# Performance work log

Measured on AMD Instinct MI355X. Metric: run time of the kernel, lower is better.

## Reference

```python
import jax, jax.numpy as jnp
import numpy as np

D_MODEL = 2048
N_HEADS = 16
HEAD_DIM = D_MODEL // N_HEADS  # 128
B, T = 2, 2048


def setup_inputs() -> dict:
    key = jax.random.key(0)
    ks = jax.random.split(key, 5)
    s = 0.02
    x = jax.random.normal(ks[0], (B, T, D_MODEL), dtype=jnp.float32)
    # weights stored as [in, out] (math-equivalent to torch Linear's W.T)
    Wq = jax.random.normal(ks[1], (D_MODEL, D_MODEL), dtype=jnp.float32) * s
    Wk = jax.random.normal(ks[2], (D_MODEL, HEAD_DIM), dtype=jnp.float32) * s
    Wv = jax.random.normal(ks[3], (D_MODEL, HEAD_DIM), dtype=jnp.float32) * s
    Wo = jax.random.normal(ks[4], (D_MODEL, D_MODEL), dtype=jnp.float32) * s
    return {"x": x, "Wq": Wq, "Wk": Wk, "Wv": Wv, "Wo": Wo}


def reference(x, Wq, Wk, Wv, Wo):
    Bx, Tx, Dx = x.shape
    scale = HEAD_DIM ** -0.5
    # q: (B, H, T, hd); k, v: single shared head (B, T, hd)
    q = (x @ Wq).reshape(Bx, Tx, N_HEADS, HEAD_DIM).transpose(0, 2, 1, 3)
    k = x @ Wk  # (B, T, hd)
    v = x @ Wv  # (B, T, hd)
    # scores: (B, H, T, T) -- shared KV head broadcast across query heads
    attn = jnp.einsum('bhqd,bkd->bhqk', q, k) * scale
    causal = jnp.triu(jnp.ones((Tx, Tx), dtype=bool), k=1)  # True = masked
    attn = jnp.where(causal[None, None], -jnp.inf, attn)
    weights = jax.nn.softmax(attn, axis=-1)
    weights = jnp.nan_to_num(weights)
    out = jnp.einsum('bhqk,bkd->bhqd', weights, v)  # (B, H, T, hd)
    out = out.transpose(0, 2, 1, 3).reshape(Bx, Tx, Dx)
    return out @ Wo
```

## Files before the change

### kernel.cpp

```cpp
#include <hip/hip_runtime.h>

typedef __bf16 bf16x8 __attribute__((ext_vector_type(8)));
typedef float f32x4 __attribute__((ext_vector_type(4)));

__device__ inline void gload16(const __bf16* g, __bf16* l) {
  __builtin_amdgcn_global_load_lds(
      (const __attribute__((address_space(1))) unsigned int*)g,
      (__attribute__((address_space(3))) unsigned int*)l, 16, 0, 0);
}

__global__ __launch_bounds__(256) void conv_bf16(
    const float* __restrict__ in, __bf16* __restrict__ out)
{
  size_t i = ((size_t)blockIdx.x * 256 + threadIdx.x) * 8;
  float4 a = *(const float4*)&in[i];
  float4 b = *(const float4*)&in[i + 4];
  bf16x8 h;
  h[0] = (__bf16)a.x; h[1] = (__bf16)a.y; h[2] = (__bf16)a.z; h[3] = (__bf16)a.w;
  h[4] = (__bf16)b.x; h[5] = (__bf16)b.y; h[6] = (__bf16)b.z; h[7] = (__bf16)b.w;
  *(bf16x8*)&out[i] = h;
}

__global__ __launch_bounds__(256) void transpose_w(
    const float* __restrict__ W, __bf16* __restrict__ WT, int Kd, int Nd)
{
  __shared__ __bf16 Ts[64 * 72];
  const int tid = threadIdx.x;
  const int c0 = blockIdx.x * 64, r0 = blockIdx.y * 64;
#pragma unroll
  for (int i = 0; i < 4; i++) {
    int row = (tid >> 4) + i * 16, cv = (tid & 15) * 4;
    float4 w = *(const float4*)&W[(size_t)(r0 + row) * Nd + c0 + cv];
    Ts[(cv + 0) * 72 + row] = (__bf16)w.x;
    Ts[(cv + 1) * 72 + row] = (__bf16)w.y;
    Ts[(cv + 2) * 72 + row] = (__bf16)w.z;
    Ts[(cv + 3) * 72 + row] = (__bf16)w.w;
  }
  __syncthreads();
#pragma unroll
  for (int i = 0; i < 4; i++) {
    int n = (tid >> 4) + i * 16, kseg = (tid & 15) * 4;
    *(uint2*)&WT[(size_t)(c0 + n) * Kd + r0 + kseg] = *(uint2*)&Ts[n * 72 + kseg];
  }
}

__global__ __launch_bounds__(256) void gemm_qkv(
    const __bf16* __restrict__ A, const __bf16* __restrict__ WqT,
    const __bf16* __restrict__ WkT, const __bf16* __restrict__ WvT,
    __bf16* __restrict__ Cq, __bf16* __restrict__ Ck, __bf16* __restrict__ Cv)
{
  __shared__ __align__(16) __bf16 Asl[128 * 32];
  __shared__ __align__(16) __bf16 Bsl[128 * 32];
  const int tid = threadIdx.x, wave = tid >> 6, lane = tid & 63;
  const int quad = lane >> 4, l16 = lane & 15;
  const int nb = blockIdx.x, m0 = blockIdx.y * 128;
  const __bf16* BT; __bf16* C; int ldC, c0;
  if (nb < 16)       { BT = WqT + (size_t)nb * 128 * 2048; C = Cq; ldC = 2048; c0 = nb * 128; }
  else if (nb == 16) { BT = WkT; C = Ck; ldC = 128; c0 = 0; }
  else               { BT = WvT; C = Cv; ldC = 128; c0 = 0; }
  const int wm = (wave >> 1) * 64, wn = (wave & 1) * 64;
  const int lrow = lane >> 2, lseg = (lane & 3) * 8;

  f32x4 acc[4][4];
#pragma unroll
  for (int i = 0; i < 4; i++)
#pragma unroll
    for (int j = 0; j < 4; j++) acc[i][j] = (f32x4){0.f, 0.f, 0.f, 0.f};

  for (int k0 = 0; k0 < 2048; k0 += 32) {
    __syncthreads();
#pragma unroll
    for (int c = 0; c < 2; c++) {
      int ch = wave * 2 + c;
      gload16(&A[(size_t)(m0 + ch * 16 + lrow) * 2048 + k0 + lseg], &Asl[ch * 512]);
      gload16(&BT[(size_t)(ch * 16 + lrow) * 2048 + k0 + lseg], &Bsl[ch * 512]);
    }
    __syncthreads();

    bf16x8 af[4], bf[4];
#pragma unroll
    for (int i = 0; i < 4; i++)
      af[i] = *(const bf16x8*)&Asl[(wm + i * 16 + l16) * 32 + quad * 8];
#pragma unroll
    for (int i = 0; i < 4; i++)
      bf[i] = *(const bf16x8*)&Bsl[(wn + i * 16 + l16) * 32 + quad * 8];
#pragma unroll
    for (int mi = 0; mi < 4; mi++)
#pragma unroll
      for (int ni = 0; ni < 4; ni++)
        acc[mi][ni] = __builtin_amdgcn_mfma_f32_16x16x32_bf16(
            af[mi], bf[ni], acc[mi][ni], 0, 0, 0);
  }

#pragma unroll
  for (int mi = 0; mi < 4; mi++)
#pragma unroll
    for (int ni = 0; ni < 4; ni++)
#pragma unroll
      for (int r = 0; r < 4; r++) {
        int row = m0 + wm + mi * 16 + quad * 4 + r;
        int col = c0 + wn + ni * 16 + l16;
        C[(size_t)row * ldC + col] = (__bf16)acc[mi][ni][r];
      }
}

__global__ __launch_bounds__(256) void gemm_out_bt(
    const __bf16* __restrict__ A, const __bf16* __restrict__ BT,
    float* __restrict__ Cp)
{
  __shared__ __align__(16) __bf16 Asl[128 * 32];
  __shared__ __align__(16) __bf16 Bsl[128 * 32];
  const int tid = threadIdx.x, wave = tid >> 6, lane = tid & 63;
  const int quad = lane >> 4, l16 = lane & 15;
  const int n0 = blockIdx.x * 128, m0 = blockIdx.y * 128;
  const int wm = (wave >> 1) * 64, wn = (wave & 1) * 64;
  const int lrow = lane >> 2, lseg = (lane & 3) * 8;

  f32x4 acc[4][4];
#pragma unroll
  for (int i = 0; i < 4; i++)
#pragma unroll
    for (int j = 0; j < 4; j++) acc[i][j] = (f32x4){0.f, 0.f, 0.f, 0.f};

  for (int k0 = 0; k0 < 2048; k0 += 32) {
    __syncthreads();
#pragma unroll
    for (int c = 0; c < 2; c++) {
      int ch = wave * 2 + c;
      gload16(&A[(size_t)(m0 + ch * 16 + lrow) * 2048 + k0 + lseg], &Asl[ch * 512]);
      gload16(&BT[(size_t)(n0 + ch * 16 + lrow) * 2048 + k0 + lseg], &Bsl[ch * 512]);
    }
    __syncthreads();

    bf16x8 af[4], bf[4];
#pragma unroll
    for (int i = 0; i < 4; i++)
      af[i] = *(const bf16x8*)&Asl[(wm + i * 16 + l16) * 32 + quad * 8];
#pragma unroll
    for (int i = 0; i < 4; i++)
      bf[i] = *(const bf16x8*)&Bsl[(wn + i * 16 + l16) * 32 + quad * 8];
#pragma unroll
    for (int mi = 0; mi < 4; mi++)
#pragma unroll
      for (int ni = 0; ni < 4; ni++)
        acc[mi][ni] = __builtin_amdgcn_mfma_f32_16x16x32_bf16(
            af[mi], bf[ni], acc[mi][ni], 0, 0, 0);
  }

#pragma unroll
  for (int mi = 0; mi < 4; mi++)
#pragma unroll
    for (int ni = 0; ni < 4; ni++)
#pragma unroll
      for (int r = 0; r < 4; r++) {
        int row = m0 + wm + mi * 16 + quad * 4 + r;
        int col = n0 + wn + ni * 16 + l16;
        Cp[(size_t)row * 2048 + col] = acc[mi][ni][r];
      }
}

__global__ __launch_bounds__(256) void gemm_out_f32b(
    const __bf16* __restrict__ A, const float* __restrict__ B,
    float* __restrict__ Cp)
{
  __shared__ __align__(16) __bf16 Asl[128 * 32];
  __shared__ __align__(16) __bf16 BsT[128 * 32];
  const int tid = threadIdx.x, wave = tid >> 6, lane = tid & 63;
  const int quad = lane >> 4, l16 = lane & 15;
  const int n0 = blockIdx.x * 128, m0 = blockIdx.y * 128;
  const int wm = (wave >> 1) * 64, wn = (wave & 1) * 64;
  const int lrow = lane >> 2, lseg = (lane & 3) * 8;
  const int kg = (tid >> 5) * 4, ng = (tid & 31) * 4;

  f32x4 acc[4][4];
#pragma unroll
  for (int i = 0; i < 4; i++)
#pragma unroll
    for (int j = 0; j < 4; j++) acc[i][j] = (f32x4){0.f, 0.f, 0.f, 0.f};

  for (int k0 = 0; k0 < 2048; k0 += 32) {
    __syncthreads();
#pragma unroll
    for (int c = 0; c < 2; c++) {
      int ch = wave * 2 + c;
      gload16(&A[(size_t)(m0 + ch * 16 + lrow) * 2048 + k0 + lseg], &Asl[ch * 512]);
    }
    __bf16 h[4][4];
#pragma unroll
    for (int i = 0; i < 4; i++) {
      float4 w = *(const float4*)&B[(size_t)(k0 + kg + i) * 2048 + n0 + ng];
      h[i][0] = (__bf16)w.x; h[i][1] = (__bf16)w.y;
      h[i][2] = (__bf16)w.z; h[i][3] = (__bf16)w.w;
    }
#pragma unroll
    for (int j = 0; j < 4; j++) {
      int n = ng + j;
      int pb = ((kg >> 3) + (n >> 2)) & 3;
      __bf16 o4[4] = {h[0][j], h[1][j], h[2][j], h[3][j]};
      *(uint2*)&BsT[n * 32 + pb * 8 + (kg & 7)] = *(uint2*)o4;
    }
    __syncthreads();

    bf16x8 af[4], bf[4];
#pragma unroll
    for (int i = 0; i < 4; i++)
      af[i] = *(const bf16x8*)&Asl[(wm + i * 16 + l16) * 32 + quad * 8];
#pragma unroll
    for (int i = 0; i < 4; i++) {
      int n = wn + i * 16 + l16;
      int pb = (quad + (n >> 2)) & 3;
      bf[i] = *(const bf16x8*)&BsT[n * 32 + pb * 8];
    }
#pragma unroll
    for (int mi = 0; mi < 4; mi++)
#pragma unroll
      for (int ni = 0; ni < 4; ni++)
        acc[mi][ni] = __builtin_amdgcn_mfma_f32_16x16x32_bf16(
            af[mi], bf[ni], acc[mi][ni], 0, 0, 0);
  }

#pragma unroll
  for (int mi = 0; mi < 4; mi++)
#pragma unroll
    for (int ni = 0; ni < 4; ni++)
#pragma unroll
      for (int r = 0; r < 4; r++) {
        int row = m0 + wm + mi * 16 + quad * 4 + r;
        int col = n0 + wn + ni * 16 + l16;
        Cp[(size_t)row * 2048 + col] = acc[mi][ni][r];
      }
}

#define KS_LD 136
#define VT_LD 72
#define PR_LD 72

__global__ __launch_bounds__(256) void mqa_attn_mfma(
    const __bf16* Q, const __bf16* __restrict__ Km,
    const __bf16* __restrict__ Vm, __bf16* O)
{
  __shared__ __align__(16) __bf16 Ks[64 * KS_LD];
  __shared__ __align__(16) __bf16 VsT[128 * VT_LD];
  __shared__ __align__(16) __bf16 Pr[4][32 * PR_LD];

  const int tid = threadIdx.x, wave = tid >> 6, lane = tid & 63;
  const int quad = lane >> 4, l16 = lane & 15;
  const int t = blockIdx.x >> 1, bat = blockIdx.x & 1;
  const int hg = blockIdx.y & 3, flip = blockIdx.y >> 2;
  const int qt = flip ? (63 - t) : t;
  const int h = hg * 4 + wave;
  const int q0 = qt * 32;
  const size_t qgrow = (size_t)bat * 2048 + q0;
  const float SCL2 = 0.08838834764831845f * 1.4426950408889634f;

  bf16x8 qf[2][4];
#pragma unroll
  for (int mi = 0; mi < 2; mi++)
#pragma unroll
    for (int ks = 0; ks < 4; ks++)
      qf[mi][ks] = *(const bf16x8*)(Q + (qgrow + mi * 16 + l16) * 2048 +
                                    h * 128 + ks * 32 + quad * 8);

  bf16x8 ones;
#pragma unroll
  for (int i = 0; i < 8; i++) ones[i] = (__bf16)1.0f;

  f32x4 oa[2][8];
#pragma unroll
  for (int mi = 0; mi < 2; mi++)
#pragma unroll
    for (int nt = 0; nt < 8; nt++) oa[mi][nt] = (f32x4){0.f, 0.f, 0.f, 0.f};
  f32x4 lacc[2];
  lacc[0] = (f32x4){0.f, 0.f, 0.f, 0.f};
  lacc[1] = (f32x4){0.f, 0.f, 0.f, 0.f};

  const __bf16* Kb = Km + (size_t)bat * 2048 * 128;
  const __bf16* Vb = Vm + (size_t)bat * 2048 * 128;
  const int qmax = q0 + 31;

  for (int sc = 0; sc <= qmax; sc += 64) {
    __syncthreads();
#pragma unroll
    for (int i = 0; i < 4; i++) {
      int v = tid + i * 256;
      int row = v >> 4, dseg = (v & 15) * 8;
      int kr = sc + row; if (kr > 2047) kr = 2047;
      *(bf16x8*)&Ks[row * KS_LD + dseg] =
          *(const bf16x8*)&Kb[(size_t)kr * 128 + dseg];
    }
#pragma unroll
    for (int i = 0; i < 2; i++) {
      int g = tid + i * 256;
      int dg = (g & 31) * 4, kg2 = (g >> 5) * 4;
      union { uint2 u; unsigned short s[4]; } a[4], o;
#pragma unroll
      for (int i2 = 0; i2 < 4; i2++) {
        int kr = sc + kg2 + i2; if (kr > 2047) kr = 2047;
        a[i2].u = *(const uint2*)&Vb[(size_t)kr * 128 + dg];
      }
#pragma unroll
      for (int j = 0; j < 4; j++) {
        int d = dg + j;
        int pb = ((kg2 >> 3) + (d >> 2)) & 7;
        o.s[0] = a[0].s[j]; o.s[1] = a[1].s[j];
        o.s[2] = a[2].s[j]; o.s[3] = a[3].s[j];
        *(uint2*)&VsT[d * VT_LD + pb * 8 + (kg2 & 7)] = o.u;
      }
    }
    __syncthreads();

    f32x4 sf[2][4];
#pragma unroll
    for (int mi = 0; mi < 2; mi++)
#pragma unroll
      for (int kt = 0; kt < 4; kt++) sf[mi][kt] = (f32x4){0.f, 0.f, 0.f, 0.f};
#pragma unroll
    for (int ks = 0; ks < 4; ks++)
#pragma unroll
      for (int kt = 0; kt < 4; kt++) {
        bf16x8 kf = *(const bf16x8*)&Ks[(kt * 16 + l16) * KS_LD + ks * 32 + quad * 8];
        sf[0][kt] = __builtin_amdgcn_mfma_f32_16x16x32_bf16(kf, qf[0][ks], sf[0][kt], 0, 0, 0);
        sf[1][kt] = __builtin_amdgcn_mfma_f32_16x16x32_bf16(kf, qf[1][ks], sf[1][kt], 0, 0, 0);
      }

    __bf16* prw = Pr[wave];
    if (sc + 64 > q0) {
#pragma unroll
      for (int mi = 0; mi < 2; mi++) {
        int qrow = q0 + mi * 16 + l16;
#pragma unroll
        for (int kt = 0; kt < 4; kt++) {
          int kbase = sc + kt * 16 + quad * 4;
          __bf16 h4[4];
#pragma unroll
          for (int r = 0; r < 4; r++) {
            float p = (kbase + r <= qrow) ? exp2f(sf[mi][kt][r] * SCL2) : 0.f;
            h4[r] = (__bf16)p;
          }
          *(uint2*)&prw[(mi * 16 + l16) * PR_LD + kt * 16 + quad * 4] = *(uint2*)h4;
        }
      }
    } else {
#pragma unroll
      for (int mi = 0; mi < 2; mi++)
#pragma unroll
        for (int kt = 0; kt < 4; kt++) {
          __bf16 h4[4];
#pragma unroll
          for (int r = 0; r < 4; r++) h4[r] = (__bf16)exp2f(sf[mi][kt][r] * SCL2);
          *(uint2*)&prw[(mi * 16 + l16) * PR_LD + kt * 16 + quad * 4] = *(uint2*)h4;
        }
    }

#pragma unroll
    for (int ks2 = 0; ks2 < 2; ks2++) {
      bf16x8 pf0 = *(const bf16x8*)&prw[(l16) * PR_LD + ks2 * 32 + quad * 8];
      bf16x8 pf1 = *(const bf16x8*)&prw[(16 + l16) * PR_LD + ks2 * 32 + quad * 8];
      lacc[0] = __builtin_amdgcn_mfma_f32_16x16x32_bf16(pf0, ones, lacc[0], 0, 0, 0);
      lacc[1] = __builtin_amdgcn_mfma_f32_16x16x32_bf16(pf1, ones, lacc[1], 0, 0, 0);
#pragma unroll
      for (int nt = 0; nt < 8; nt++) {
        int d = nt * 16 + l16;
        int pb = ((ks2 * 4 + quad) + (d >> 2)) & 7;
        bf16x8 vf = *(const bf16x8*)&VsT[d * VT_LD + pb * 8];
        oa[0][nt] = __builtin_amdgcn_mfma_f32_16x16x32_bf16(pf0, vf, oa[0][nt], 0, 0, 0);
        oa[1][nt] = __builtin_amdgcn_mfma_f32_16x16x32_bf16(pf1, vf, oa[1][nt], 0, 0, 0);
      }
    }
  }

#pragma unroll
  for (int mi = 0; mi < 2; mi++)
#pragma unroll
    for (int r = 0; r < 4; r++) {
      float inv = 1.f / lacc[mi][r];
      size_t row = qgrow + mi * 16 + quad * 4 + r;
#pragma unroll
      for (int nt = 0; nt < 8; nt++)
        O[row * 2048 + h * 128 + nt * 16 + l16] = (__bf16)(oa[mi][nt][r] * inv);
    }
}

extern "C" void kernel_launch(void* const* d_in, const int* in_sizes, int n_in,
                              void* d_out, int out_size, void* d_ws, size_t ws_size,
                              hipStream_t stream) {
  const float* x  = (const float*)d_in[0];
  const float* Wq = (const float*)d_in[1];
  const float* Wk = (const float*)d_in[2];
  const float* Wv = (const float*)d_in[3];
  const float* Wo = (const float*)d_in[4];
  float* out = (float*)d_out;

  __bf16* q   = (__bf16*)d_ws;
  __bf16* WoT = (__bf16*)((char*)d_ws + 16777216);
  const bool have_wot = ws_size >= (size_t)(16777216 + 8388608);

  char* ob = (char*)d_out;
  __bf16* xb  = (__bf16*)(ob);
  __bf16* WqT = (__bf16*)(ob + 16777216);
  __bf16* WkT = (__bf16*)(ob + 25165824);
  __bf16* WvT = (__bf16*)(ob + 25690112);
  __bf16* kb  = (__bf16*)(ob + 26214400);
  __bf16* vb  = (__bf16*)(ob + 27262976);

  dim3 blk(256);
  conv_bf16<<<4096, blk, 0, stream>>>(x, xb);
  transpose_w<<<dim3(32, 32), blk, 0, stream>>>(Wq, WqT, 2048, 2048);
  transpose_w<<<dim3(2, 32), blk, 0, stream>>>(Wk, WkT, 2048, 128);
  transpose_w<<<dim3(2, 32), blk, 0, stream>>>(Wv, WvT, 2048, 128);
  if (have_wot)
    transpose_w<<<dim3(32, 32), blk, 0, stream>>>(Wo, WoT, 2048, 2048);
  gemm_qkv<<<dim3(18, 32), blk, 0, stream>>>(xb, WqT, WkT, WvT, q, kb, vb);
  mqa_attn_mfma<<<dim3(64, 8, 1), blk, 0, stream>>>(q, kb, vb, q);
  if (have_wot)
    gemm_out_bt<<<dim3(16, 32), blk, 0, stream>>>(q, WoT, out);
  else
    gemm_out_f32b<<<dim3(16, 32), blk, 0, stream>>>(q, Wo, out);
}
```

Baseline: 298.2 us.

## Double-buffer K via async global-to-LDS loads and prefetch V in attention loop

The attention kernel now double-buffers the K tile in LDS, issuing the next chunk with global_load_lds DMA, and uses an XOR-swizzled unpadded layout in place of row padding. V for the next chunk is loaded into registers during compute and transposed into LDS after it. This is meant to hide global-memory latency behind the QK and PV MFMA work. Launch bounds now request two blocks per CU, which raises LDS use and register pressure and adds an extra barrier per iteration.

```diff
diff --git a/kernel.cpp b/kernel.cpp
--- a/kernel.cpp
+++ b/kernel.cpp
@@ -231,15 +231,14 @@
       }
 }
 
-#define KS_LD 136
 #define VT_LD 72
 #define PR_LD 72
 
-__global__ __launch_bounds__(256) void mqa_attn_mfma(
+__global__ __launch_bounds__(256, 2) void mqa_attn_mfma(
     const __bf16* Q, const __bf16* __restrict__ Km,
     const __bf16* __restrict__ Vm, __bf16* O)
 {
-  __shared__ __align__(16) __bf16 Ks[64 * KS_LD];
+  __shared__ __align__(16) __bf16 Ks[2][64 * 128];
   __shared__ __align__(16) __bf16 VsT[128 * VT_LD];
   __shared__ __align__(16) __bf16 Pr[4][32 * PR_LD];
 
@@ -277,37 +276,66 @@
   const __bf16* Kb = Km + (size_t)bat * 2048 * 128;
   const __bf16* Vb = Vm + (size_t)bat * 2048 * 128;
   const int qmax = q0 + 31;
-
-  for (int sc = 0; sc <= qmax; sc += 64) {
-    __syncthreads();
-#pragma unroll
-    for (int i = 0; i < 4; i++) {
-      int v = tid + i * 256;
-      int row = v >> 4, dseg = (v & 15) * 8;
-      int kr = sc + row; if (kr > 2047) kr = 2047;
-      *(bf16x8*)&Ks[row * KS_LD + dseg] =
-          *(const bf16x8*)&Kb[(size_t)kr * 128 + dseg];
-    }
-#pragma unroll
-    for (int i = 0; i < 2; i++) {
-      int g = tid + i * 256;
-      int dg = (g & 31) * 4, kg2 = (g >> 5) * 4;
-      union { uint2 u; unsigned short s[4]; } a[4], o;
-#pragma unroll
-      for (int i2 = 0; i2 < 4; i2++) {
-        int kr = sc + kg2 + i2; if (kr > 2047) kr = 2047;
-        a[i2].u = *(const uint2*)&Vb[(size_t)kr * 128 + dg];
-      }
-#pragma unroll
-      for (int j = 0; j < 4; j++) {
-        int d = dg + j;
-        int pb = ((kg2 >> 3) + (d >> 2)) & 7;
-        o.s[0] = a[0].s[j]; o.s[1] = a[1].s[j];
-        o.s[2] = a[2].s[j]; o.s[3] = a[3].s[j];
-        *(uint2*)&VsT[d * VT_LD + pb * 8 + (kg2 & 7)] = o.u;
-      }
-    }
-    __syncthreads();
+  const int nch = (qmax >> 6) + 1;
+
+  size_t koff[4];
+#pragma unroll
+  for (int p = 0; p < 4; p++) {
+    int row = wave * 16 + p * 4 + (lane >> 4);
+    int dbs = (lane & 15) ^ (row & 7);
+    koff[p] = (size_t)row * 128 + (size_t)dbs * 8;
+  }
+  int kswz[4];
+#pragma unroll
+  for (int ks = 0; ks < 4; ks++)
+    kswz[ks] = (((ks << 2) | quad) ^ (l16 & 7)) << 3;
+  const int vdg = (tid & 31) * 4;
+  const int vkgA = (tid >> 5) * 4;
+  uint2 va[2][4];
+
+#define ISSUE_K(Kc, buf)                                                     \
+  {                                                                          \
+    _Pragma("unroll") for (int p = 0; p < 4; p++)                            \
+        gload16((Kc) + koff[p], &Ks[buf][(wave * 4 + p) * 512]);             \
+  }
+#define LOAD_V(Vc)                                                           \
+  {                                                                          \
+    _Pragma("unroll") for (int i = 0; i < 2; i++)                            \
+        _Pragma("unroll") for (int r = 0; r < 4; r++)                        \
+            va[i][r] =                                                       \
+        *(const uint2*)&(Vc)[(size_t)(vkgA + i * 32 + r) * 128 + vdg];       \
+  }
+#define WRITE_V()                                                            \
+  {                                                                          \
+    _Pragma("unroll") for (int i = 0; i < 2; i++) {                          \
+      int kg2 = vkgA + i * 32;                                               \
+      _Pragma("unroll") for (int j = 0; j < 4; j++) {                        \
+        int d = vdg + j;                                                     \
+        int pb = ((kg2 >> 3) + (d >> 2)) & 7;                                \
+        union { uint2 u; unsigned short s[4]; } o;                           \
+        o.s[0] = ((const unsigned short*)&va[i][0])[j];                      \
+        o.s[1] = ((const unsigned short*)&va[i][1])[j];                      \
+        o.s[2] = ((const unsigned short*)&va[i][2])[j];                      \
+        o.s[3] = ((const unsigned short*)&va[i][3])[j];                      \
+        *(uint2*)&VsT[d * VT_LD + pb * 8 + (kg2 & 7)] = o.u;                 \
+      }                                                                      \
+    }                                                                        \
+  }
+
+  ISSUE_K(Kb, 0);
+  LOAD_V(Vb);
+  WRITE_V();
+  __syncthreads();
+
+  for (int c = 0; c < nch; ++c) {
+    const int sc = c << 6;
+    const __bf16* Ksb = Ks[c & 1];
+    const bool pf = (c + 1 < nch);
+
+    if (pf) {
+      ISSUE_K(Kb + (size_t)(sc + 64) * 128, (c & 1) ^ 1);
+      LOAD_V(Vb + (size_t)(sc + 64) * 128);
+    }
 
     f32x4 sf[2][4];
 #pragma unroll
@@ -318,7 +346,7 @@
     for (int ks = 0; ks < 4; ks++)
 #pragma unroll
       for (int kt = 0; kt < 4; kt++) {
-        bf16x8 kf = *(const bf16x8*)&Ks[(kt * 16 + l16) * KS_LD + ks * 32 + quad * 8];
+        bf16x8 kf = *(const bf16x8*)&Ksb[(kt * 16 + l16) * 128 + kswz[ks]];
         sf[0][kt] = __builtin_amdgcn_mfma_f32_16x16x32_bf16(kf, qf[0][ks], sf[0][kt], 0, 0, 0);
         sf[1][kt] = __builtin_amdgcn_mfma_f32_16x16x32_bf16(kf, qf[1][ks], sf[1][kt], 0, 0, 0);
       }
@@ -367,6 +395,12 @@
         oa[1][nt] = __builtin_amdgcn_mfma_f32_16x16x32_bf16(pf1, vf, oa[1][nt], 0, 0, 0);
       }
     }
+
+    if (pf) {
+      __syncthreads();
+      WRITE_V();
+      __syncthreads();
+    }
   }
 
 #pragma unroll
@@ -379,6 +413,9 @@
       for (int nt = 0; nt < 8; nt++)
         O[row * 2048 + h * 128 + nt * 16 + l16] = (__bf16)(oa[mi][nt][r] * inv);
     }
+#undef ISSUE_K
+#undef LOAD_V
+#undef WRITE_V
 }
 
 extern "C" void kernel_launch(void* const* d_in, const int* in_sizes, int n_in,
```

After: 296.0 us. No clear change (-0.7%).

## Split long causal attention tiles across two blocks and merge partials

Applied to the files above, without the earlier changes.

Query tiles in the second half of the sequence, which have the most causal KV chunks, are each split into two blocks that process half the chunks. This shortens the longest blocks and spreads work over more blocks. The first half writes fp32 partial outputs and row sums into reused scratch in the output buffer. The second half writes unnormalized bf16 partials, and a new combine kernel sums them and normalizes. The change also adds a launch-bounds occupancy hint and an extra launch, and rounding the unnormalized partial to bf16 before the merge may cost a little precision.

```diff
diff --git a/kernel.cpp b/kernel.cpp
--- a/kernel.cpp
+++ b/kernel.cpp
@@ -235,9 +235,10 @@
 #define VT_LD 72
 #define PR_LD 72
 
-__global__ __launch_bounds__(256) void mqa_attn_mfma(
+__global__ __launch_bounds__(256, 3) void mqa_attn_mfma(
     const __bf16* Q, const __bf16* __restrict__ Km,
-    const __bf16* __restrict__ Vm, __bf16* O)
+    const __bf16* __restrict__ Vm, __bf16* O,
+    float* __restrict__ Oacc, float* __restrict__ Lp)
 {
   __shared__ __align__(16) __bf16 Ks[64 * KS_LD];
   __shared__ __align__(16) __bf16 VsT[128 * VT_LD];
@@ -245,14 +246,26 @@
 
   const int tid = threadIdx.x, wave = tid >> 6, lane = tid & 63;
   const int quad = lane >> 4, l16 = lane & 15;
-  const int t = blockIdx.x >> 1, bat = blockIdx.x & 1;
-  const int hg = blockIdx.y & 3, flip = blockIdx.y >> 2;
-  const int qt = flip ? (63 - t) : t;
+  const int bx = blockIdx.x;
+  int qt, half, split;
+  if (bx < 64) { split = 1; qt = 63 - (bx >> 1); half = bx & 1; }
+  else         { split = 0; qt = 95 - bx; half = 1; }
+  const int hg = blockIdx.y & 3, bat = blockIdx.y >> 2;
   const int h = hg * 4 + wave;
   const int q0 = qt * 32;
   const size_t qgrow = (size_t)bat * 2048 + q0;
   const float SCL2 = 0.08838834764831845f * 1.4426950408889634f;
 
+  const int nch = (qt >> 1) + 1;
+  int cbeg, cend;
+  if (split) {
+    int nh = nch >> 1;
+    cbeg = half ? nh : 0;
+    cend = half ? nch : nh;
+  } else {
+    cbeg = 0; cend = nch;
+  }
+
   bf16x8 qf[2][4];
 #pragma unroll
   for (int mi = 0; mi < 2; mi++)
@@ -276,9 +289,9 @@
 
   const __bf16* Kb = Km + (size_t)bat * 2048 * 128;
   const __bf16* Vb = Vm + (size_t)bat * 2048 * 128;
-  const int qmax = q0 + 31;
-
-  for (int sc = 0; sc <= qmax; sc += 64) {
+
+  for (int c = cbeg; c < cend; ++c) {
+    const int sc = c << 6;
     __syncthreads();
 #pragma unroll
     for (int i = 0; i < 4; i++) {
@@ -369,16 +382,81 @@
     }
   }
 
-#pragma unroll
-  for (int mi = 0; mi < 2; mi++)
-#pragma unroll
-    for (int r = 0; r < 4; r++) {
-      float inv = 1.f / lacc[mi][r];
-      size_t row = qgrow + mi * 16 + quad * 4 + r;
-#pragma unroll
-      for (int nt = 0; nt < 8; nt++)
-        O[row * 2048 + h * 128 + nt * 16 + l16] = (__bf16)(oa[mi][nt][r] * inv);
-    }
+  if (!split) {
+#pragma unroll
+    for (int mi = 0; mi < 2; mi++)
+#pragma unroll
+      for (int r = 0; r < 4; r++) {
+        float inv = 1.f / lacc[mi][r];
+        size_t row = qgrow + mi * 16 + quad * 4 + r;
+#pragma unroll
+        for (int nt = 0; nt < 8; nt++)
+          O[row * 2048 + h * 128 + nt * 16 + l16] = (__bf16)(oa[mi][nt][r] * inv);
+      }
+  } else if (half == 1) {
+#pragma unroll
+    for (int mi = 0; mi < 2; mi++)
+#pragma unroll
+      for (int r = 0; r < 4; r++) {
+        size_t row = qgrow + mi * 16 + quad * 4 + r;
+#pragma unroll
+        for (int nt = 0; nt < 8; nt++)
+          O[row * 2048 + h * 128 + nt * 16 + l16] = (__bf16)oa[mi][nt][r];
+      }
+    if (l16 == 0) {
+#pragma unroll
+      for (int mi = 0; mi < 2; mi++)
+#pragma unroll
+        for (int r = 0; r < 4; r++)
+          Lp[((size_t)(2 + bat) * 1024 + (q0 - 1024) + mi * 16 + quad * 4 + r) * 16 + h] =
+              lacc[mi][r];
+    }
+  } else {
+    float* Ob = Oacc + ((size_t)bat * 1024 + (q0 - 1024)) * 2048 + h * 128;
+#pragma unroll
+    for (int mi = 0; mi < 2; mi++)
+#pragma unroll
+      for (int r = 0; r < 4; r++) {
+        int ro = (mi * 16 + quad * 4 + r) * 2048;
+#pragma unroll
+        for (int nt = 0; nt < 8; nt++)
+          Ob[ro + nt * 16 + l16] = oa[mi][nt][r];
+      }
+    if (l16 == 0) {
+#pragma unroll
+      for (int mi = 0; mi < 2; mi++)
+#pragma unroll
+        for (int r = 0; r < 4; r++)
+          Lp[((size_t)bat * 1024 + (q0 - 1024) + mi * 16 + quad * 4 + r) * 16 + h] =
+              lacc[mi][r];
+    }
+  }
+}
+
+__global__ __launch_bounds__(256) void attn_combine(
+    const float* __restrict__ Oacc, const float* __restrict__ Lp,
+    __bf16* __restrict__ O)
+{
+  const int bat = blockIdx.x >> 10, row1k = blockIdx.x & 1023;
+  const int col = threadIdx.x * 8, h = threadIdx.x >> 4;
+  const float l0 = Lp[((size_t)bat * 1024 + row1k) * 16 + h];
+  const float l1 = Lp[((size_t)(2 + bat) * 1024 + row1k) * 16 + h];
+  const float inv = 1.f / (l0 + l1);
+  const float* oap = &Oacc[((size_t)bat * 1024 + row1k) * 2048 + col];
+  float4 a = *(const float4*)oap;
+  float4 b = *(const float4*)(oap + 4);
+  __bf16* op = &O[((size_t)bat * 2048 + 1024 + row1k) * 2048 + col];
+  bf16x8 p = *(const bf16x8*)op;
+  bf16x8 o;
+  o[0] = (__bf16)((a.x + (float)p[0]) * inv);
+  o[1] = (__bf16)((a.y + (float)p[1]) * inv);
+  o[2] = (__bf16)((a.z + (float)p[2]) * inv);
+  o[3] = (__bf16)((a.w + (float)p[3]) * inv);
+  o[4] = (__bf16)((b.x + (float)p[4]) * inv);
+  o[5] = (__bf16)((b.y + (float)p[5]) * inv);
+  o[6] = (__bf16)((b.z + (float)p[6]) * inv);
+  o[7] = (__bf16)((b.w + (float)p[7]) * inv);
+  *(bf16x8*)op = o;
 }
 
 extern "C" void kernel_launch(void* const* d_in, const int* in_sizes, int n_in,
@@ -403,6 +481,9 @@
   __bf16* kb  = (__bf16*)(ob + 26214400);
   __bf16* vb  = (__bf16*)(ob + 27262976);
 
+  float* Oacc = (float*)xb;
+  float* Lp   = (float*)WkT;
+
   dim3 blk(256);
   conv_bf16<<<4096, blk, 0, stream>>>(x, xb);
   transpose_w<<<dim3(32, 32), blk, 0, stream>>>(Wq, WqT, 2048, 2048);
@@ -411,7 +492,8 @@
   if (have_wot)
     transpose_w<<<dim3(32, 32), blk, 0, stream>>>(Wo, WoT, 2048, 2048);
   gemm_qkv<<<dim3(18, 32), blk, 0, stream>>>(xb, WqT, WkT, WvT, q, kb, vb);
-  mqa_attn_mfma<<<dim3(64, 8, 1), blk, 0, stream>>>(q, kb, vb, q);
+  mqa_attn_mfma<<<dim3(96, 8, 1), blk, 0, stream>>>(q, kb, vb, q, Oacc, Lp);
+  attn_combine<<<2048, blk, 0, stream>>>(Oacc, Lp, q);
   if (have_wot)
     gemm_out_bt<<<dim3(16, 32), blk, 0, stream>>>(q, WoT, out);
   else
```

Result: slower. 404.8 us (+35.7%).

## Triple-buffer QKV and output GEMMs with 128x256 tiles and block swizzle

Applied to the files above, without the earlier changes.

Both bf16 GEMMs move to 512-thread blocks computing 128x256 tiles. They use a three-stage LDS ring filled by async global-to-LDS loads, with explicit vmcnt waits and a single barrier per k-step. This replaces the load/sync/compute/sync loop and is meant to overlap memory latency with MFMA work. In the QKV GEMM, K and V are computed as one 256-wide tile, which relies on WkT and WvT being laid out contiguously. Block indices are remapped for L2 locality. The cost is about 72KB of LDS per block, which lowers occupancy.

```diff
diff --git a/kernel.cpp b/kernel.cpp
--- a/kernel.cpp
+++ b/kernel.cpp
@@ -2,6 +2,8 @@
 
 typedef __bf16 bf16x8 __attribute__((ext_vector_type(8)));
 typedef float f32x4 __attribute__((ext_vector_type(4)));
+
+#define VMCNT(n) asm volatile("s_waitcnt vmcnt(" #n ")" ::: "memory")
 
 __device__ inline void gload16(const __bf16* g, __bf16* l) {
   __builtin_amdgcn_global_load_lds(
@@ -44,108 +46,155 @@
   }
 }
 
-__global__ __launch_bounds__(256) void gemm_qkv(
+__global__ __launch_bounds__(512) void gemm_qkv(
     const __bf16* __restrict__ A, const __bf16* __restrict__ WqT,
     const __bf16* __restrict__ WkT, const __bf16* __restrict__ WvT,
     __bf16* __restrict__ Cq, __bf16* __restrict__ Ck, __bf16* __restrict__ Cv)
 {
-  __shared__ __align__(16) __bf16 Asl[128 * 32];
-  __shared__ __align__(16) __bf16 Bsl[128 * 32];
+  __shared__ __align__(16) __bf16 Asl[3][128 * 32];
+  __shared__ __align__(16) __bf16 Bsl[3][256 * 32];
   const int tid = threadIdx.x, wave = tid >> 6, lane = tid & 63;
   const int quad = lane >> 4, l16 = lane & 15;
-  const int nb = blockIdx.x, m0 = blockIdx.y * 128;
-  const __bf16* BT; __bf16* C; int ldC, c0;
-  if (nb < 16)       { BT = WqT + (size_t)nb * 128 * 2048; C = Cq; ldC = 2048; c0 = nb * 128; }
-  else if (nb == 16) { BT = WkT; C = Ck; ldC = 128; c0 = 0; }
-  else               { BT = WvT; C = Cv; ldC = 128; c0 = 0; }
-  const int wm = (wave >> 1) * 64, wn = (wave & 1) * 64;
+  int bid = blockIdx.x + 9 * blockIdx.y;
+  bid = (bid & 7) * 36 + (bid >> 3);
+  const int p = bid % 9, m0 = (bid / 9) * 128;
+  const __bf16* BT = (p < 8) ? (WqT + (size_t)p * 256 * 2048) : WkT;
+  const int wm = (wave & 1) * 64, wn = (wave >> 1) * 64;
   const int lrow = lane >> 2, lseg = (lane & 3) * 8;
 
+  const size_t aRow  = (size_t)(m0 + wave * 16 + lrow) * 2048 + lseg;
+  const size_t bRow0 = (size_t)(wave * 16 + lrow) * 2048 + lseg;
+  const size_t bRow1 = (size_t)((wave + 8) * 16 + lrow) * 2048 + lseg;
+
+#define STAGE_Q(T, B)                                                      \
+  {                                                                        \
+    gload16(&A[aRow + (size_t)(T) * 32], &Asl[B][wave * 512]);             \
+    gload16(&BT[bRow0 + (size_t)(T) * 32], &Bsl[B][wave * 512]);           \
+    gload16(&BT[bRow1 + (size_t)(T) * 32], &Bsl[B][(wave + 8) * 512]);     \
+  }
+
   f32x4 acc[4][4];
 #pragma unroll
   for (int i = 0; i < 4; i++)
 #pragma unroll
     for (int j = 0; j < 4; j++) acc[i][j] = (f32x4){0.f, 0.f, 0.f, 0.f};
 
-  for (int k0 = 0; k0 < 2048; k0 += 32) {
-    __syncthreads();
-#pragma unroll
-    for (int c = 0; c < 2; c++) {
-      int ch = wave * 2 + c;
-      gload16(&A[(size_t)(m0 + ch * 16 + lrow) * 2048 + k0 + lseg], &Asl[ch * 512]);
-      gload16(&BT[(size_t)(ch * 16 + lrow) * 2048 + k0 + lseg], &Bsl[ch * 512]);
-    }
-    __syncthreads();
+  STAGE_Q(0, 0);
+  STAGE_Q(1, 1);
+  VMCNT(3);
+  __builtin_amdgcn_s_barrier();
+
+  int cur = 0;
+  for (int t = 0; t < 64; ++t) {
+    const int nxt = (cur == 0) ? 2 : cur - 1;
+    if (t + 2 < 64) STAGE_Q(t + 2, nxt);
 
     bf16x8 af[4], bf[4];
 #pragma unroll
     for (int i = 0; i < 4; i++)
-      af[i] = *(const bf16x8*)&Asl[(wm + i * 16 + l16) * 32 + quad * 8];
+      af[i] = *(const bf16x8*)&Asl[cur][(wm + i * 16 + l16) * 32 + quad * 8];
 #pragma unroll
     for (int i = 0; i < 4; i++)
-      bf[i] = *(const bf16x8*)&Bsl[(wn + i * 16 + l16) * 32 + quad * 8];
+      bf[i] = *(const bf16x8*)&Bsl[cur][(wn + i * 16 + l16) * 32 + quad * 8];
 #pragma unroll
     for (int mi = 0; mi < 4; mi++)
 #pragma unroll
       for (int ni = 0; ni < 4; ni++)
         acc[mi][ni] = __builtin_amdgcn_mfma_f32_16x16x32_bf16(
             af[mi], bf[ni], acc[mi][ni], 0, 0, 0);
-  }
-
-#pragma unroll
-  for (int mi = 0; mi < 4; mi++)
-#pragma unroll
-    for (int ni = 0; ni < 4; ni++)
-#pragma unroll
-      for (int r = 0; r < 4; r++) {
-        int row = m0 + wm + mi * 16 + quad * 4 + r;
-        int col = c0 + wn + ni * 16 + l16;
-        C[(size_t)row * ldC + col] = (__bf16)acc[mi][ni][r];
-      }
-}
-
-__global__ __launch_bounds__(256) void gemm_out_bt(
+
+    if (t + 2 < 64)      { VMCNT(3); __builtin_amdgcn_s_barrier(); }
+    else if (t + 1 < 64) { VMCNT(0); __builtin_amdgcn_s_barrier(); }
+    cur = (cur == 2) ? 0 : cur + 1;
+  }
+#undef STAGE_Q
+
+  if (p < 8) {
+#pragma unroll
+    for (int mi = 0; mi < 4; mi++)
+#pragma unroll
+      for (int ni = 0; ni < 4; ni++)
+#pragma unroll
+        for (int r = 0; r < 4; r++) {
+          int row = m0 + wm + mi * 16 + quad * 4 + r;
+          int col = p * 256 + wn + ni * 16 + l16;
+          Cq[(size_t)row * 2048 + col] = (__bf16)acc[mi][ni][r];
+        }
+  } else {
+#pragma unroll
+    for (int mi = 0; mi < 4; mi++)
+#pragma unroll
+      for (int ni = 0; ni < 4; ni++)
+#pragma unroll
+        for (int r = 0; r < 4; r++) {
+          int row = m0 + wm + mi * 16 + quad * 4 + r;
+          int col = wn + ni * 16 + l16;
+          if (col < 128) Ck[(size_t)row * 128 + col] = (__bf16)acc[mi][ni][r];
+          else           Cv[(size_t)row * 128 + (col - 128)] = (__bf16)acc[mi][ni][r];
+        }
+  }
+}
+
+__global__ __launch_bounds__(512) void gemm_out_bt(
     const __bf16* __restrict__ A, const __bf16* __restrict__ BT,
     float* __restrict__ Cp)
 {
-  __shared__ __align__(16) __bf16 Asl[128 * 32];
-  __shared__ __align__(16) __bf16 Bsl[128 * 32];
+  __shared__ __align__(16) __bf16 Asl[3][128 * 32];
+  __shared__ __align__(16) __bf16 Bsl[3][256 * 32];
   const int tid = threadIdx.x, wave = tid >> 6, lane = tid & 63;
   const int quad = lane >> 4, l16 = lane & 15;
-  const int n0 = blockIdx.x * 128, m0 = blockIdx.y * 128;
-  const int wm = (wave >> 1) * 64, wn = (wave & 1) * 64;
+  int bid = blockIdx.x + 8 * blockIdx.y;
+  bid = (bid & 7) * 32 + (bid >> 3);
+  const int n0 = (bid % 8) * 256, m0 = (bid / 8) * 128;
+  const int wm = (wave & 1) * 64, wn = (wave >> 1) * 64;
   const int lrow = lane >> 2, lseg = (lane & 3) * 8;
 
+  const size_t aRow  = (size_t)(m0 + wave * 16 + lrow) * 2048 + lseg;
+  const size_t bRow0 = (size_t)(n0 + wave * 16 + lrow) * 2048 + lseg;
+  const size_t bRow1 = (size_t)(n0 + (wave + 8) * 16 + lrow) * 2048 + lseg;
+
+#define STAGE_O(T, B)                                                      \
+  {                                                                        \
+    gload16(&A[aRow + (size_t)(T) * 32], &Asl[B][wave * 512]);             \
+    gload16(&BT[bRow0 + (size_t)(T) * 32], &Bsl[B][wave * 512]);           \
+    gload16(&BT[bRow1 + (size_t)(T) * 32], &Bsl[B][(wave + 8) * 512]);     \
+  }
+
   f32x4 acc[4][4];
 #pragma unroll
   for (int i = 0; i < 4; i++)
 #pragma unroll
     for (int j = 0; j < 4; j++) acc[i][j] = (f32x4){0.f, 0.f, 0.f, 0.f};
 
-  for (int k0 = 0; k0 < 2048; k0 += 32) {
-    __syncthreads();
-#pragma unroll
-    for (int c = 0; c < 2; c++) {
-      int ch = wave * 2 + c;
-      gload16(&A[(size_t)(m0 + ch * 16 + lrow) * 2048 + k0 + lseg], &Asl[ch * 512]);
-      gload16(&BT[(size_t)(n0 + ch * 16 + lrow) * 2048 + k0 + lseg], &Bsl[ch * 512]);
-    }
-    __syncthreads();
+  STAGE_O(0, 0);
+  STAGE_O(1, 1);
+  VMCNT(3);
+  __builtin_amdgcn_s_barrier();
+
+  int cur = 0;
+  for (int t = 0; t < 64; ++t) {
+    const int nxt = (cur == 0) ? 2 : cur - 1;
+    if (t + 2 < 64) STAGE_O(t + 2, nxt);
 
     bf16x8 af[4], bf[4];
 #pragma unroll
     for (int i = 0; i < 4; i++)
-      af[i] = *(const bf16x8*)&Asl[(wm + i * 16 + l16) * 32 + quad * 8];
+      af[i] = *(const bf16x8*)&Asl[cur][(wm + i * 16 + l16) * 32 + quad * 8];
 #pragma unroll
     for (int i = 0; i < 4; i++)
-      bf[i] = *(const bf16x8*)&Bsl[(wn + i * 16 + l16) * 32 + quad * 8];
+      bf[i] = *(const bf16x8*)&Bsl[cur][(wn + i * 16 + l16) * 32 + quad * 8];
 #pragma unroll
     for (int mi = 0; mi < 4; mi++)
 #pragma unroll
       for (int ni = 0; ni < 4; ni++)
         acc[mi][ni] = __builtin_amdgcn_mfma_f32_16x16x32_bf16(
             af[mi], bf[ni], acc[mi][ni], 0, 0, 0);
-  }
+
+    if (t + 2 < 64)      { VMCNT(3); __builtin_amdgcn_s_barrier(); }
+    else if (t + 1 < 64) { VMCNT(0); __builtin_amdgcn_s_barrier(); }
+    cur = (cur == 2) ? 0 : cur + 1;
+  }
+#undef STAGE_O
 
 #pragma unroll
   for (int mi = 0; mi < 4; mi++)
@@ -410,10 +459,10 @@
   transpose_w<<<dim3(2, 32), blk, 0, stream>>>(Wv, WvT, 2048, 128);
   if (have_wot)
     transpose_w<<<dim3(32, 32), blk, 0, stream>>>(Wo, WoT, 2048, 2048);
-  gemm_qkv<<<dim3(18, 32), blk, 0, stream>>>(xb, WqT, WkT, WvT, q, kb, vb);
+  gemm_qkv<<<dim3(9, 32), dim3(512), 0, stream>>>(xb, WqT, WkT, WvT, q, kb, vb);
   mqa_attn_mfma<<<dim3(64, 8, 1), blk, 0, stream>>>(q, kb, vb, q);
   if (have_wot)
-    gemm_out_bt<<<dim3(16, 32), blk, 0, stream>>>(q, WoT, out);
+    gemm_out_bt<<<dim3(8, 32), dim3(512), 0, stream>>>(q, WoT, out);
   else
     gemm_out_f32b<<<dim3(16, 32), blk, 0, stream>>>(q, Wo, out);
 }
```

Result: no change. 303.5 us (+1.8%).
